# Kernel tuning notes

Measured on AMD Instinct MI355X. Metric: run time of the kernel, lower is better.

Reference implementation:

```python
import jax, jax.numpy as jnp
import numpy as np

NEG = -1e30  # effective -inf, safe under logaddexp


def _rna_loss(logits, targets, fbank_len, text_len, blank=0):
    """RNA loss: forward lattice DP over (T, U).

    logits: [B, T, U, V] raw scores (U = max_labels + 1)
    targets: [B, U-1] int labels; fbank_len/text_len: [B] int lengths.
    Each frame emits exactly one symbol (blank -> stay at u, label -> u+1).
    """
    log_probs = jax.nn.log_softmax(logits, axis=-1)          # [B,T,U,V]
    B, T, U, V = logits.shape
    L = U - 1
    lab = targets.astype(jnp.int32)                          # [B,L]
    lp_blank = jnp.transpose(log_probs[..., blank], (1, 0, 2))   # [T,B,U]
    # prob of emitting label u+1 while at state u: gather target token
    lp_label = jnp.take_along_axis(
        log_probs[:, :, :L, :], lab[:, None, :, None], axis=3)[..., 0]  # [B,T,L]
    lp_label = jnp.transpose(lp_label, (1, 0, 2))            # [T,B,L]

    alpha0 = jnp.full((B, U), NEG, dtype=log_probs.dtype).at[:, 0].set(0.0)

    def step(alpha, xs):
        lpb, lpl = xs                                        # [B,U], [B,L]
        stay = alpha + lpb                                   # emit blank
        move = jnp.pad(alpha[:, :L] + lpl, ((0, 0), (1, 0)),
                       constant_values=NEG)                  # emit label
        new = jnp.logaddexp(stay, move)
        return new, new

    _, alphas = jax.lax.scan(step, alpha0, (lp_blank, lp_label))  # [T,B,U]
    alphas = jnp.concatenate([alpha0[None], alphas], axis=0)      # [T+1,B,U]
    ll = alphas[fbank_len, jnp.arange(B), text_len]               # [B]
    return -ll


def setup_inputs() -> dict:
    key = jax.random.key(0)
    k1, k2, k3, k4 = jax.random.split(key, 4)
    B, T, L, V = 4, 512, 64, 1024
    logits = jax.random.normal(k1, (B, T, L + 1, V), dtype=jnp.float32)
    targets = jax.random.randint(k2, (B, L), 1, V, dtype=jnp.int32)
    fbank_len = jax.random.randint(k3, (B,), 384, T + 1, dtype=jnp.int32)
    text_len = jax.random.randint(k4, (B,), 32, L + 1, dtype=jnp.int32)
    return {"logits": logits, "targets": targets,
            "fbank_len": fbank_len, "text_len": text_len}


def reference(logits, targets, fbank_len, text_len):
    loss = _rna_loss(logits, targets, fbank_len, text_len, blank=0)
    return loss.mean()  # reduction='mean'
```

## Files before the change

kernel.cpp:

```cpp
#include <hip/hip_runtime.h>

#define NEGF (-1e30f)

namespace {

constexpr int B = 4, T = 512, L = 64, U = 65, V = 1024;

__device__ __forceinline__ float lse2(float a, float b) {
    float m = fmaxf(a, b);
    float d = fminf(a, b) - m;
    return m + __logf(1.0f + __expf(d));
}

__global__ __launch_bounds__(256) void rna_lse_kernel(
    const float* __restrict__ logits, const int* __restrict__ targets,
    const int* __restrict__ fbank_len, const int* __restrict__ text_len,
    float* __restrict__ lpb, float* __restrict__ lpl) {
    const int lane = threadIdx.x & 63;
    const int row  = blockIdx.x * 4 + (threadIdx.x >> 6);
    const int u  = row % U;
    const int bt = row / U;
    const int t  = bt % T;
    const int b  = bt / T;

    const int fb = fbank_len[b];
    const int tl = text_len[b];
    if (t >= fb || u > tl || u > t + 1 || (tl - u) > (fb - t)) return;

    const float*  p  = logits + (size_t)row * V;
    const float4* p4 = (const float4*)p;
    float4 v0 = p4[lane];
    float4 v1 = p4[lane + 64];
    float4 v2 = p4[lane + 128];
    float4 v3 = p4[lane + 192];

    float m = fmaxf(fmaxf(fmaxf(v0.x, v0.y), fmaxf(v0.z, v0.w)),
              fmaxf(fmaxf(fmaxf(v1.x, v1.y), fmaxf(v1.z, v1.w)),
              fmaxf(fmaxf(fmaxf(v2.x, v2.y), fmaxf(v2.z, v2.w)),
                    fmaxf(fmaxf(v3.x, v3.y), fmaxf(v3.z, v3.w)))));
#pragma unroll
    for (int off = 32; off > 0; off >>= 1)
        m = fmaxf(m, __shfl_xor(m, off, 64));

    float s = __expf(v0.x - m) + __expf(v0.y - m) + __expf(v0.z - m) + __expf(v0.w - m)
            + __expf(v1.x - m) + __expf(v1.y - m) + __expf(v1.z - m) + __expf(v1.w - m)
            + __expf(v2.x - m) + __expf(v2.y - m) + __expf(v2.z - m) + __expf(v2.w - m)
            + __expf(v3.x - m) + __expf(v3.y - m) + __expf(v3.z - m) + __expf(v3.w - m);
#pragma unroll
    for (int off = 32; off > 0; off >>= 1)
        s += __shfl_xor(s, off, 64);

    if (lane == 0) {
        float lse = m + __logf(s);
        lpb[(b * U + u) * T + t] = v0.x - lse;
        if (u < L) {
            int tgt = targets[b * L + u];
            lpl[(b * U + u + 1) * T + t] = p[tgt] - lse;
        }
    }
}

__global__ __launch_bounds__(256) void rna_dp_kernel(
    const float* __restrict__ lpb, const float* __restrict__ lpl,
    const int* __restrict__ fbank_len, const int* __restrict__ text_len,
    float* __restrict__ out) {
    __shared__ float res[B];
    const int lane = threadIdx.x & 63;
    const int b    = threadIdx.x >> 6;
    const int fb   = fbank_len[b];
    const int tl   = text_len[b];

    const float* pbR   = lpb + (b * U + lane) * T;
    const float* plR   = lpl + (b * U + lane) * T;
    const float* pbR64 = lpb + (b * U + 64) * T;
    const float* plR64 = lpl + (b * U + 64) * T;

    float alpha   = (lane == 0) ? 0.0f : NEGF;
    float alpha64 = NEGF;

    float cb[8], cl[8], cb64[8], cl64[8];
    {
        float4 a0 = *(const float4*)(pbR);     float4 a1 = *(const float4*)(pbR + 4);
        cb[0]=a0.x; cb[1]=a0.y; cb[2]=a0.z; cb[3]=a0.w;
        cb[4]=a1.x; cb[5]=a1.y; cb[6]=a1.z; cb[7]=a1.w;
        float4 b0 = *(const float4*)(plR);     float4 b1 = *(const float4*)(plR + 4);
        cl[0]=b0.x; cl[1]=b0.y; cl[2]=b0.z; cl[3]=b0.w;
        cl[4]=b1.x; cl[5]=b1.y; cl[6]=b1.z; cl[7]=b1.w;
        float4 c0 = *(const float4*)(pbR64);   float4 c1 = *(const float4*)(pbR64 + 4);
        cb64[0]=c0.x; cb64[1]=c0.y; cb64[2]=c0.z; cb64[3]=c0.w;
        cb64[4]=c1.x; cb64[5]=c1.y; cb64[6]=c1.z; cb64[7]=c1.w;
        float4 d0 = *(const float4*)(plR64);   float4 d1 = *(const float4*)(plR64 + 4);
        cl64[0]=d0.x; cl64[1]=d0.y; cl64[2]=d0.z; cl64[3]=d0.w;
        cl64[4]=d1.x; cl64[5]=d1.y; cl64[6]=d1.z; cl64[7]=d1.w;
    }

    for (int t0 = 0; t0 < fb; t0 += 8) {
        float nb[8], nl[8], nb64[8], nl64[8];
        const bool pf = (t0 + 8 < fb);
        if (pf) {
            const int tn = t0 + 8;
            float4 a0 = *(const float4*)(pbR + tn);   float4 a1 = *(const float4*)(pbR + tn + 4);
            nb[0]=a0.x; nb[1]=a0.y; nb[2]=a0.z; nb[3]=a0.w;
            nb[4]=a1.x; nb[5]=a1.y; nb[6]=a1.z; nb[7]=a1.w;
            float4 b0 = *(const float4*)(plR + tn);   float4 b1 = *(const float4*)(plR + tn + 4);
            nl[0]=b0.x; nl[1]=b0.y; nl[2]=b0.z; nl[3]=b0.w;
            nl[4]=b1.x; nl[5]=b1.y; nl[6]=b1.z; nl[7]=b1.w;
            float4 c0 = *(const float4*)(pbR64 + tn); float4 c1 = *(const float4*)(pbR64 + tn + 4);
            nb64[0]=c0.x; nb64[1]=c0.y; nb64[2]=c0.z; nb64[3]=c0.w;
            nb64[4]=c1.x; nb64[5]=c1.y; nb64[6]=c1.z; nb64[7]=c1.w;
            float4 d0 = *(const float4*)(plR64 + tn); float4 d1 = *(const float4*)(plR64 + tn + 4);
            nl64[0]=d0.x; nl64[1]=d0.y; nl64[2]=d0.z; nl64[3]=d0.w;
            nl64[4]=d1.x; nl64[5]=d1.y; nl64[6]=d1.z; nl64[7]=d1.w;
        }
#pragma unroll
        for (int j = 0; j < 8; ++j) {
            if (t0 + j >= fb) break;
            const int t = t0 + j;
            float ap   = __shfl_up(alpha, 1, 64);
            float stay = alpha + cb[j];
            float move = (lane == 0) ? NEGF : (ap + cl[j]);
            float na   = lse2(stay, move);
            float stay64 = alpha64 + cb64[j];
            float move64 = alpha + cl64[j];
            alpha64 = lse2(stay64, move64);
            alpha   = na;
            if (lane > t + 1) alpha = NEGF;
            if (t + 1 < 64)   alpha64 = NEGF;
        }
        if (pf) {
#pragma unroll
            for (int j = 0; j < 8; ++j) {
                cb[j] = nb[j]; cl[j] = nl[j]; cb64[j] = nb64[j]; cl64[j] = nl64[j];
            }
        }
    }

    float ans = (tl < 64) ? __shfl(alpha, tl, 64) : __shfl(alpha64, 63, 64);
    if (lane == 0) res[b] = ans;
    __syncthreads();
    if (threadIdx.x == 0)
        out[0] = -(res[0] + res[1] + res[2] + res[3]) * (1.0f / B);
}

}

extern "C" void kernel_launch(void* const* d_in, const int* in_sizes, int n_in,
                              void* d_out, int out_size, void* d_ws, size_t ws_size,
                              hipStream_t stream) {
    const float* logits  = (const float*)d_in[0];
    const int*   targets = (const int*)d_in[1];
    const int*   fbl     = (const int*)d_in[2];
    const int*   txl     = (const int*)d_in[3];
    float* lpb = (float*)d_ws;
    float* lpl = lpb + (size_t)B * U * T;
    float* out = (float*)d_out;

    const int rows = B * T * U;
    rna_lse_kernel<<<rows / 4, 256, 0, stream>>>(logits, targets, fbl, txl, lpb, lpl);
    rna_dp_kernel<<<1, 256, 0, stream>>>(lpb, lpl, fbl, txl, out);
}
```

Measured before the change: 720.5 us.

## Fuse LSE and DP kernels with atomic counters so the DP overlaps production

Merges the log-softmax producer and the serial DP into one launch. Block 0 runs the DP and spin-waits on per-batch, per-8-frame atomic counters that producer blocks increment with release semantics once their rows are written. The goal is to overlap the long serial DP chain with the bandwidth-bound logit streaming instead of running them back to back. In exchange it adds a small kernel to clear the counters, atomics on every row, and a reliance on block 0 being resident while the other blocks run.

```diff
diff --git a/kernel.cpp b/kernel.cpp
--- a/kernel.cpp
+++ b/kernel.cpp
@@ -12,105 +12,121 @@
     return m + __logf(1.0f + __expf(d));
 }
 
-__global__ __launch_bounds__(256) void rna_lse_kernel(
+#define LOAD8(dst, p, tn) do {                                        \
+    float4 _a = *(const float4*)((p) + (tn));                         \
+    float4 _b = *(const float4*)((p) + (tn) + 4);                     \
+    dst[0]=_a.x; dst[1]=_a.y; dst[2]=_a.z; dst[3]=_a.w;               \
+    dst[4]=_b.x; dst[5]=_b.y; dst[6]=_b.z; dst[7]=_b.w;               \
+} while (0)
+
+__global__ void rna_clear_kernel(int* __restrict__ ctr) {
+    ctr[threadIdx.x] = 0;
+}
+
+__global__ __launch_bounds__(256) void rna_fused_kernel(
     const float* __restrict__ logits, const int* __restrict__ targets,
     const int* __restrict__ fbank_len, const int* __restrict__ text_len,
-    float* __restrict__ lpb, float* __restrict__ lpl) {
+    float* __restrict__ lpb, float* __restrict__ lpl,
+    int* __restrict__ ctr, float* __restrict__ out) {
+
     const int lane = threadIdx.x & 63;
-    const int row  = blockIdx.x * 4 + (threadIdx.x >> 6);
-    const int u  = row % U;
-    const int bt = row / U;
-    const int t  = bt % T;
-    const int b  = bt / T;
 
+    if (blockIdx.x != 0) {
+        const int row  = (blockIdx.x - 1) * 4 + (threadIdx.x >> 6);
+        const int u  = row % U;
+        const int bt = row / U;
+        const int t  = bt % T;
+        const int b  = bt / T;
+
+        const int fb = fbank_len[b];
+        const int tl = text_len[b];
+        if (t >= fb || u > tl || u > t + 1 || (tl - u) > (fb - t)) return;
+
+        const float*  p  = logits + (size_t)row * V;
+        const float4* p4 = (const float4*)p;
+        float4 v0 = p4[lane];
+        float4 v1 = p4[lane + 64];
+        float4 v2 = p4[lane + 128];
+        float4 v3 = p4[lane + 192];
+
+        float m = fmaxf(fmaxf(fmaxf(v0.x, v0.y), fmaxf(v0.z, v0.w)),
+                  fmaxf(fmaxf(fmaxf(v1.x, v1.y), fmaxf(v1.z, v1.w)),
+                  fmaxf(fmaxf(fmaxf(v2.x, v2.y), fmaxf(v2.z, v2.w)),
+                        fmaxf(fmaxf(v3.x, v3.y), fmaxf(v3.z, v3.w)))));
+#pragma unroll
+        for (int off = 32; off > 0; off >>= 1)
+            m = fmaxf(m, __shfl_xor(m, off, 64));
+
+        float s = __expf(v0.x - m) + __expf(v0.y - m) + __expf(v0.z - m) + __expf(v0.w - m)
+                + __expf(v1.x - m) + __expf(v1.y - m) + __expf(v1.z - m) + __expf(v1.w - m)
+                + __expf(v2.x - m) + __expf(v2.y - m) + __expf(v2.z - m) + __expf(v2.w - m)
+                + __expf(v3.x - m) + __expf(v3.y - m) + __expf(v3.z - m) + __expf(v3.w - m);
+#pragma unroll
+        for (int off = 32; off > 0; off >>= 1)
+            s += __shfl_xor(s, off, 64);
+
+        if (lane == 0) {
+            float lse = m + __logf(s);
+            lpb[(b * U + u) * T + t] = v0.x - lse;
+            if (u < L) {
+                int tgt = targets[b * L + u];
+                lpl[(b * U + u + 1) * T + t] = p[tgt] - lse;
+            }
+            __hip_atomic_fetch_add(&ctr[b * 64 + (t >> 3)], 1,
+                                   __ATOMIC_RELEASE, __HIP_MEMORY_SCOPE_AGENT);
+        }
+        return;
+    }
+
+    __shared__ float res[B];
+    const int b  = threadIdx.x >> 6;
     const int fb = fbank_len[b];
     const int tl = text_len[b];
-    if (t >= fb || u > tl || u > t + 1 || (tl - u) > (fb - t)) return;
-
-    const float*  p  = logits + (size_t)row * V;
-    const float4* p4 = (const float4*)p;
-    float4 v0 = p4[lane];
-    float4 v1 = p4[lane + 64];
-    float4 v2 = p4[lane + 128];
-    float4 v3 = p4[lane + 192];
-
-    float m = fmaxf(fmaxf(fmaxf(v0.x, v0.y), fmaxf(v0.z, v0.w)),
-              fmaxf(fmaxf(fmaxf(v1.x, v1.y), fmaxf(v1.z, v1.w)),
-              fmaxf(fmaxf(fmaxf(v2.x, v2.y), fmaxf(v2.z, v2.w)),
-                    fmaxf(fmaxf(v3.x, v3.y), fmaxf(v3.z, v3.w)))));
-#pragma unroll
-    for (int off = 32; off > 0; off >>= 1)
-        m = fmaxf(m, __shfl_xor(m, off, 64));
-
-    float s = __expf(v0.x - m) + __expf(v0.y - m) + __expf(v0.z - m) + __expf(v0.w - m)
-            + __expf(v1.x - m) + __expf(v1.y - m) + __expf(v1.z - m) + __expf(v1.w - m)
-            + __expf(v2.x - m) + __expf(v2.y - m) + __expf(v2.z - m) + __expf(v2.w - m)
-            + __expf(v3.x - m) + __expf(v3.y - m) + __expf(v3.z - m) + __expf(v3.w - m);
-#pragma unroll
-    for (int off = 32; off > 0; off >>= 1)
-        s += __shfl_xor(s, off, 64);
-
-    if (lane == 0) {
-        float lse = m + __logf(s);
-        lpb[(b * U + u) * T + t] = v0.x - lse;
-        if (u < L) {
-            int tgt = targets[b * L + u];
-            lpl[(b * U + u + 1) * T + t] = p[tgt] - lse;
-        }
-    }
-}
-
-__global__ __launch_bounds__(256) void rna_dp_kernel(
-    const float* __restrict__ lpb, const float* __restrict__ lpl,
-    const int* __restrict__ fbank_len, const int* __restrict__ text_len,
-    float* __restrict__ out) {
-    __shared__ float res[B];
-    const int lane = threadIdx.x & 63;
-    const int b    = threadIdx.x >> 6;
-    const int fb   = fbank_len[b];
-    const int tl   = text_len[b];
 
     const float* pbR   = lpb + (b * U + lane) * T;
     const float* plR   = lpl + (b * U + lane) * T;
     const float* pbR64 = lpb + (b * U + 64) * T;
     const float* plR64 = lpl + (b * U + 64) * T;
+    const int*   myctr = ctr + b * 64;
+
+    auto grp_expect = [&](int g) -> int {
+        int e = 0;
+#pragma unroll
+        for (int j = 0; j < 8; ++j) {
+            int t = g * 8 + j;
+            if (t < fb) {
+                int hi = min(tl, t + 1);
+                int lo = max(0, tl - (fb - t));
+                e += hi - lo + 1;
+            }
+        }
+        return e;
+    };
+    auto wait_grp = [&](int g) {
+        const int expect = grp_expect(g);
+        while (__hip_atomic_load(&myctr[g], __ATOMIC_ACQUIRE,
+                                 __HIP_MEMORY_SCOPE_AGENT) < expect) {
+            __builtin_amdgcn_s_sleep(2);
+        }
+    };
 
     float alpha   = (lane == 0) ? 0.0f : NEGF;
     float alpha64 = NEGF;
 
     float cb[8], cl[8], cb64[8], cl64[8];
-    {
-        float4 a0 = *(const float4*)(pbR);     float4 a1 = *(const float4*)(pbR + 4);
-        cb[0]=a0.x; cb[1]=a0.y; cb[2]=a0.z; cb[3]=a0.w;
-        cb[4]=a1.x; cb[5]=a1.y; cb[6]=a1.z; cb[7]=a1.w;
-        float4 b0 = *(const float4*)(plR);     float4 b1 = *(const float4*)(plR + 4);
-        cl[0]=b0.x; cl[1]=b0.y; cl[2]=b0.z; cl[3]=b0.w;
-        cl[4]=b1.x; cl[5]=b1.y; cl[6]=b1.z; cl[7]=b1.w;
-        float4 c0 = *(const float4*)(pbR64);   float4 c1 = *(const float4*)(pbR64 + 4);
-        cb64[0]=c0.x; cb64[1]=c0.y; cb64[2]=c0.z; cb64[3]=c0.w;
-        cb64[4]=c1.x; cb64[5]=c1.y; cb64[6]=c1.z; cb64[7]=c1.w;
-        float4 d0 = *(const float4*)(plR64);   float4 d1 = *(const float4*)(plR64 + 4);
-        cl64[0]=d0.x; cl64[1]=d0.y; cl64[2]=d0.z; cl64[3]=d0.w;
-        cl64[4]=d1.x; cl64[5]=d1.y; cl64[6]=d1.z; cl64[7]=d1.w;
-    }
+    float nb[8], nl[8], nb64[8], nl64[8];
+
+    wait_grp(0);
+    LOAD8(cb,   pbR,   0); LOAD8(cl,   plR,   0);
+    LOAD8(cb64, pbR64, 0); LOAD8(cl64, plR64, 0);
 
     for (int t0 = 0; t0 < fb; t0 += 8) {
-        float nb[8], nl[8], nb64[8], nl64[8];
         const bool pf = (t0 + 8 < fb);
         if (pf) {
+            wait_grp((t0 >> 3) + 1);
             const int tn = t0 + 8;
-            float4 a0 = *(const float4*)(pbR + tn);   float4 a1 = *(const float4*)(pbR + tn + 4);
-            nb[0]=a0.x; nb[1]=a0.y; nb[2]=a0.z; nb[3]=a0.w;
-            nb[4]=a1.x; nb[5]=a1.y; nb[6]=a1.z; nb[7]=a1.w;
-            float4 b0 = *(const float4*)(plR + tn);   float4 b1 = *(const float4*)(plR + tn + 4);
-            nl[0]=b0.x; nl[1]=b0.y; nl[2]=b0.z; nl[3]=b0.w;
-            nl[4]=b1.x; nl[5]=b1.y; nl[6]=b1.z; nl[7]=b1.w;
-            float4 c0 = *(const float4*)(pbR64 + tn); float4 c1 = *(const float4*)(pbR64 + tn + 4);
-            nb64[0]=c0.x; nb64[1]=c0.y; nb64[2]=c0.z; nb64[3]=c0.w;
-            nb64[4]=c1.x; nb64[5]=c1.y; nb64[6]=c1.z; nb64[7]=c1.w;
-            float4 d0 = *(const float4*)(plR64 + tn); float4 d1 = *(const float4*)(plR64 + tn + 4);
-            nl64[0]=d0.x; nl64[1]=d0.y; nl64[2]=d0.z; nl64[3]=d0.w;
-            nl64[4]=d1.x; nl64[5]=d1.y; nl64[6]=d1.z; nl64[7]=d1.w;
+            LOAD8(nb,   pbR,   tn); LOAD8(nl,   plR,   tn);
+            LOAD8(nb64, pbR64, tn); LOAD8(nl64, plR64, tn);
         }
 #pragma unroll
         for (int j = 0; j < 8; ++j) {
@@ -153,9 +169,11 @@
     const int*   txl     = (const int*)d_in[3];
     float* lpb = (float*)d_ws;
     float* lpl = lpb + (size_t)B * U * T;
+    int*   ctr = (int*)(lpl + (size_t)B * U * T);
     float* out = (float*)d_out;
 
+    rna_clear_kernel<<<1, B * 64, 0, stream>>>(ctr);
     const int rows = B * T * U;
-    rna_lse_kernel<<<rows / 4, 256, 0, stream>>>(logits, targets, fbl, txl, lpb, lpl);
-    rna_dp_kernel<<<1, 256, 0, stream>>>(lpb, lpl, fbl, txl, out);
+    rna_fused_kernel<<<rows / 4 + 1, 256, 0, stream>>>(
+        logits, targets, fbl, txl, lpb, lpl, ctr, out);
 }
```

After: 2.441 ms. 239% more time.
